# Kernel optimization log

Hardware: AMD Instinct MI355X
Metric: run time of the kernel (lower is better)

Reference implementation:

```python
import jax, jax.numpy as jnp
import numpy as np

B, S, H = 1, 2048, 4096
NQ, NKV, D = 32, 8, 128
N_REP = NQ // NKV
SCALE = 1.0 / np.sqrt(D)
SOFTCAP = 30.0
EPS = 1e-5


def _rotate_half(x):
    x1, x2 = jnp.split(x, 2, axis=-1)
    return jnp.concatenate([-x2, x1], axis=-1)


def _rms_norm(x, w, eps=EPS):
    xf = x.astype(jnp.float32)
    norm = xf * jax.lax.rsqrt(jnp.mean(xf * xf, axis=-1, keepdims=True) + eps)
    return (w * norm).astype(x.dtype)


def setup_inputs() -> dict:
    key = jax.random.key(0)
    ks = jax.random.split(key, 8)
    hidden_states = jax.random.normal(ks[0], (B, S, H), dtype=jnp.float32)
    # causal additive mask
    causal = jnp.tril(jnp.ones((S, S), dtype=bool))
    attention_mask = jnp.where(causal, 0.0, -1e9)[None, None].astype(jnp.float32)
    # RoPE cache
    inv_freq = 1.0 / (10000.0 ** (np.arange(0, D, 2, dtype=np.float32) / D))
    t = np.arange(S, dtype=np.float32)
    freqs = np.outer(t, inv_freq)                      # (S, D/2)
    emb = np.concatenate([freqs, freqs], axis=-1)      # (S, D)
    cos = jnp.asarray(np.cos(emb))[None, None]         # (1,1,S,D)
    sin = jnp.asarray(np.sin(emb))[None, None]
    # params
    std = 0.02
    wq = jax.random.normal(ks[1], (NQ * D, H), dtype=jnp.float32) * std
    wk = jax.random.normal(ks[2], (NKV * D, H), dtype=jnp.float32) * std
    wv = jax.random.normal(ks[3], (NKV * D, H), dtype=jnp.float32) * std
    wo = jax.random.normal(ks[4], (H, NQ * D), dtype=jnp.float32) * std
    pre_norm_w = jnp.ones((H,), dtype=jnp.float32)
    q_norm_w = jnp.ones((D,), dtype=jnp.float32)
    k_norm_w = jnp.ones((D,), dtype=jnp.float32)
    return {
        "hidden_states": hidden_states, "attention_mask": attention_mask,
        "cos": cos, "sin": sin, "pre_norm_w": pre_norm_w,
        "wq": wq, "wk": wk, "wv": wv, "wo": wo,
        "q_norm_w": q_norm_w, "k_norm_w": k_norm_w,
    }


def reference(hidden_states, attention_mask, cos, sin, pre_norm_w,
              wq, wk, wv, wo, q_norm_w, k_norm_w):
    residual = hidden_states
    h = _rms_norm(hidden_states, pre_norm_w)
    bsz, seq_len, _ = h.shape
    # projections -> (b, heads, s, d)
    q = jnp.einsum('bsh,eh->bse', h, wq).reshape(bsz, seq_len, NQ, D).transpose(0, 2, 1, 3)
    k = jnp.einsum('bsh,eh->bse', h, wk).reshape(bsz, seq_len, NKV, D).transpose(0, 2, 1, 3)
    v = jnp.einsum('bsh,eh->bse', h, wv).reshape(bsz, seq_len, NKV, D).transpose(0, 2, 1, 3)
    # QK RMSNorm over head_dim
    q = _rms_norm(q, q_norm_w)
    k = _rms_norm(k, k_norm_w)
    # RoPE (full head_dim)
    q = q * cos + _rotate_half(q) * sin
    k = k * cos + _rotate_half(k) * sin
    # GQA: repeat kv heads
    k_exp = jnp.repeat(k, N_REP, axis=1)  # (b, NQ, s, d)
    v_exp = jnp.repeat(v, N_REP, axis=1)
    scores = jnp.einsum('bhqd,bhkd->bhqk', q, k_exp) * SCALE
    scores = SOFTCAP * jnp.tanh(scores / SOFTCAP)
    scores = scores + attention_mask
    probs = jax.nn.softmax(scores.astype(jnp.float32), axis=-1).astype(q.dtype)
    attn = jnp.einsum('bhqk,bhkd->bhqd', probs, v_exp)
    attn = attn.transpose(0, 2, 1, 3).reshape(bsz, seq_len, NQ * D)
    out = jnp.einsum('bse,he->bsh', attn, wo)
    return residual + out
```

## Files before the change

### kernel.cpp

```cpp
#include <hip/hip_runtime.h>
#include <cstdint>

typedef __bf16 bf16;
typedef __bf16 bf16x8 __attribute__((ext_vector_type(8)));
typedef __bf16 bf16x4 __attribute__((ext_vector_type(4)));
typedef float  f32x4  __attribute__((ext_vector_type(4)));

#define SEQ  2048
#define HID  4096
#define DH   128
#define NQH  32
#define NKVH 8
#define NTOT 6144
#define RSCALE 0.08838834764831845f
#define SOFTCAP 30.0f
#define L2E 1.4426950408889634f

__device__ __forceinline__ void gl2lds16(const void* g, void* l) {
  __builtin_amdgcn_global_load_lds(
      (const __attribute__((address_space(1))) unsigned int*)g,
      (__attribute__((address_space(3))) unsigned int*)l, 16, 0, 0);
}

__global__ void cvt_kernel(const float* __restrict__ in, bf16* __restrict__ out, int n4) {
  const int stride = gridDim.x * blockDim.x;
  for (int i = blockIdx.x * blockDim.x + threadIdx.x; i < n4; i += stride) {
    const float4 v = ((const float4*)in)[i];
    bf16x4 o = { (bf16)v.x, (bf16)v.y, (bf16)v.z, (bf16)v.w };
    *(bf16x4*)(out + (size_t)i * 4) = o;
  }
}

__global__ void rmsnorm_kernel(const float* __restrict__ x, const float* __restrict__ w,
                               bf16* __restrict__ out, float* __restrict__ res_out) {
  const int s = blockIdx.x;
  const float* xr = x + (size_t)s * HID;
  float4 v[4];
  float ss = 0.f;
#pragma unroll
  for (int j = 0; j < 4; ++j) {
    v[j] = ((const float4*)xr)[threadIdx.x + j * 256];
    ss += v[j].x * v[j].x + v[j].y * v[j].y + v[j].z * v[j].z + v[j].w * v[j].w;
  }
#pragma unroll
  for (int m = 1; m < 64; m <<= 1) ss += __shfl_xor(ss, m);
  __shared__ float red[4];
  if ((threadIdx.x & 63) == 0) red[threadIdx.x >> 6] = ss;
  __syncthreads();
  const float rn = rsqrtf((red[0] + red[1] + red[2] + red[3]) * (1.f / HID) + 1e-5f);
  bf16* orow = out + (size_t)s * HID;
  float4* rrow = (float4*)(res_out + (size_t)s * HID);
#pragma unroll
  for (int j = 0; j < 4; ++j) {
    const int idx = (threadIdx.x + j * 256) * 4;
    const float4 wv = ((const float4*)w)[threadIdx.x + j * 256];
    bf16x4 o = { (bf16)(v[j].x * rn * wv.x), (bf16)(v[j].y * rn * wv.y),
                 (bf16)(v[j].z * rn * wv.z), (bf16)(v[j].w * rn * wv.w) };
    *(bf16x4*)(orow + idx) = o;
    rrow[threadIdx.x + j * 256] = v[j];
  }
}

template<bool FINAL>
__global__ __launch_bounds__(512, 1)
void gemmring(const bf16* __restrict__ A, const bf16* __restrict__ B,
              bf16* __restrict__ Cb, float* __restrict__ Cf,
              int M, int N, int Ktot, int Klen)
{
  extern __shared__ char smem[];
  const int tid  = threadIdx.x;
  const int lane = tid & 63;
  const int wave = tid >> 6;
  const int wm = wave >> 2, wn = wave & 3;

  const int gx = gridDim.x;
  const int nwg = gx * gridDim.y;
  int lin = blockIdx.x + gx * blockIdx.y;
  lin = (lin & 7) * (nwg >> 3) + (lin >> 3);
  const int m0 = (lin / gx) * 256;
  const int n0 = (lin % gx) * 256;
  const int k0 = blockIdx.z * Klen;

  const int rsub = lane >> 2;
  const int g8   = (((lane & 3) ^ (rsub & 3))) * 8;
  auto stage = [&](int c, int sl) {
    const int kt = k0 + c * 32;
    char* base = smem + sl * 32768;
#pragma unroll
    for (int l = 0; l < 2; ++l) {
      const int p = wave * 2 + l;
      gl2lds16(A + (size_t)(m0 + p * 16 + rsub) * Ktot + kt + g8, base + p * 1024);
    }
#pragma unroll
    for (int l = 0; l < 2; ++l) {
      const int p = wave * 2 + l;
      gl2lds16(B + (size_t)(n0 + p * 16 + rsub) * Ktot + kt + g8, base + 16384 + p * 1024);
    }
  };

  f32x4 acc[8][4] = {};
  const int n_ch = Klen / 32;

  const int rl = lane & 15;
  const int sw = ((lane >> 4) ^ (lane & 3)) * 8;

  stage(0, 0); stage(1, 1); stage(2, 2); stage(3, 3);
  asm volatile("s_waitcnt vmcnt(12)" ::: "memory");
  asm volatile("s_barrier" ::: "memory");

  int rs = 0, ss = 4;
  for (int c = 0; c < n_ch; ++c) {
    if (c + 4 < n_ch) stage(c + 4, ss);
    const bf16* Ab = (const bf16*)(smem + rs * 32768);
    const bf16* Bb = (const bf16*)(smem + rs * 32768 + 16384);
    bf16x8 afr[8], bfr[4];
#pragma unroll
    for (int mi = 0; mi < 8; ++mi)
      afr[mi] = *(const bf16x8*)(Ab + (wm * 128 + mi * 16 + rl) * 32 + sw);
#pragma unroll
    for (int ni = 0; ni < 4; ++ni)
      bfr[ni] = *(const bf16x8*)(Bb + (wn * 64 + ni * 16 + rl) * 32 + sw);
    asm volatile("s_waitcnt lgkmcnt(0)" ::: "memory");
    __builtin_amdgcn_sched_barrier(0);
    __builtin_amdgcn_s_setprio(1);
#pragma unroll
    for (int mi = 0; mi < 8; ++mi)
#pragma unroll
      for (int ni = 0; ni < 4; ++ni)
        acc[mi][ni] = __builtin_amdgcn_mfma_f32_16x16x32_bf16(afr[mi], bfr[ni], acc[mi][ni], 0, 0, 0);
    __builtin_amdgcn_s_setprio(0);
    if (c + 5 <= n_ch)      { asm volatile("s_waitcnt vmcnt(12)" ::: "memory"); }
    else if (c + 4 == n_ch) { asm volatile("s_waitcnt vmcnt(8)"  ::: "memory"); }
    else if (c + 3 == n_ch) { asm volatile("s_waitcnt vmcnt(4)"  ::: "memory"); }
    else if (c + 2 == n_ch) { asm volatile("s_waitcnt vmcnt(0)"  ::: "memory"); }
    asm volatile("s_barrier" ::: "memory");
    rs = (rs == 4) ? 0 : rs + 1;
    ss = (ss == 4) ? 0 : ss + 1;
  }

#pragma unroll
  for (int mi = 0; mi < 8; ++mi) {
#pragma unroll
    for (int i = 0; i < 4; ++i) {
      const int m = m0 + wm * 128 + mi * 16 + (lane >> 4) * 4 + i;
#pragma unroll
      for (int ni = 0; ni < 4; ++ni) {
        const int n = n0 + wn * 64 + ni * 16 + (lane & 15);
        const float v = acc[mi][ni][i];
        if constexpr (FINAL) {
          atomicAdd(Cf + (size_t)m * N + n, v);
        } else {
          Cb[(size_t)m * N + n] = (bf16)v;
        }
      }
    }
  }
}

__global__ void qkrope_kernel(const bf16* __restrict__ qkv,
                              const float* __restrict__ qw, const float* __restrict__ kw,
                              const float* __restrict__ cs, const float* __restrict__ sn,
                              bf16* __restrict__ qr, bf16* __restrict__ kr)
{
  const int w = blockIdx.x * 4 + (threadIdx.x >> 6);
  const int lane = threadIdx.x & 63;
  const int s = w / (NQH + NKVH);
  const int hh = w % (NQH + NKVH);
  const bf16* src; bf16* dst; const float* nw;
  if (hh < NQH) {
    src = qkv + (size_t)s * NTOT + hh * DH;
    dst = qr + ((size_t)hh * SEQ + s) * DH;
    nw = qw;
  } else {
    const int h2 = hh - NQH;
    src = qkv + (size_t)s * NTOT + 4096 + h2 * DH;
    dst = kr + ((size_t)h2 * SEQ + s) * DH;
    nw = kw;
  }
  const float x0 = (float)src[lane], x1 = (float)src[lane + 64];
  float ss = x0 * x0 + x1 * x1;
#pragma unroll
  for (int m = 1; m < 64; m <<= 1) ss += __shfl_xor(ss, m);
  const float rn = rsqrtf(ss * (1.f / DH) + 1e-5f);
  const float n0 = x0 * rn * nw[lane], n1 = x1 * rn * nw[lane + 64];
  const float c0 = cs[s * DH + lane],      s0 = sn[s * DH + lane];
  const float c1 = cs[s * DH + lane + 64], s1 = sn[s * DH + lane + 64];
  dst[lane]      = (bf16)(n0 * c0 - n1 * s0);
  dst[lane + 64] = (bf16)(n1 * c1 + n0 * s1);
}

__global__ void vtrans_kernel(const bf16* __restrict__ qkv, bf16* __restrict__ vt)
{
  __shared__ bf16 tbuf[64][33];
  const int s0 = blockIdx.x * 64;
  const int d0 = blockIdx.y * 32;
  const int h  = blockIdx.z;
  const int tid = threadIdx.x;
  {
    const int col = tid & 31, r0 = tid >> 5;
    for (int r = r0; r < 64; r += 8)
      tbuf[r][col] = qkv[(size_t)(s0 + r) * NTOT + 5120 + h * DH + d0 + col];
  }
  __syncthreads();
  {
    const int sc = tid & 63, dr0 = tid >> 6;
    for (int d = dr0; d < 32; d += 4)
      vt[((size_t)h * DH + d0 + d) * SEQ + s0 + sc] = tbuf[sc][d];
  }
}

__global__ __launch_bounds__(256, 2)
void attn_kernel(const bf16* __restrict__ Q, const bf16* __restrict__ Kr,
                 const bf16* __restrict__ Vt, bf16* __restrict__ Oa)
{
  __shared__ bf16 Ks[2][64 * 128];
  __shared__ bf16 Vs[2][128 * 64];
  __shared__ bf16 Ps[4][32 * 64];

  const int tid = threadIdx.x, lane = tid & 63, wave = tid >> 6;

  const int lin  = blockIdx.x + 16 * blockIdx.y;
  const int slot = lin >> 8, idx = lin & 255;
  const int bx   = slot ? (15 - (idx & 15)) : (idx & 15);
  const int head = (slot << 4) | (idx >> 4);
  const int kvh  = head >> 2;
  const int q0   = bx * 128;
  const int wq0  = q0 + wave * 32;

  const bf16* Qh = Q  + (size_t)head * SEQ * DH;
  const bf16* Kh = Kr + (size_t)kvh * SEQ * DH;
  const bf16* Vh = Vt + (size_t)kvh * DH * SEQ;

  bf16x8 qf[2][4];
#pragma unroll
  for (int mt = 0; mt < 2; ++mt)
#pragma unroll
    for (int kc = 0; kc < 4; ++kc) {
      const int r = wq0 + mt * 16 + (lane & 15);
      qf[mt][kc] = *(const bf16x8*)(Qh + (size_t)r * DH + kc * 32 + (lane >> 4) * 8);
    }

  float lsum[2][4] = {};
  f32x4 o_acc[2][8] = {};

  const int ntiles = q0 / 64 + 2;

  auto stage = [&](int t, int b) {
    const int kv0 = t * 64;
    bf16* Kd = &Ks[b][0];
    bf16* Vd = &Vs[b][0];
#pragma unroll
    for (int i2 = 0; i2 < 4; ++i2) {
      const int c = wave * 4 + i2;
      {
        const int row = c * 4 + (lane >> 4);
        const int col8 = (lane & 15) ^ (row & 15);
        gl2lds16(Kh + (size_t)(kv0 + row) * DH + col8 * 8, Kd + c * 512);
      }
      {
        const int row = c * 8 + (lane >> 3);
        const int col8 = (lane & 7) ^ (row & 7);
        gl2lds16(Vh + (size_t)row * SEQ + kv0 + col8 * 8, Vd + c * 512);
      }
    }
  };

  stage(0, 0);
  __syncthreads();

  const float ZS = RSCALE / SOFTCAP;
  const float A1 = RSCALE * L2E;
  const float B3 = -(ZS * ZS) * (1.f / 3.f);
  const float B5 = (2.f / 15.f) * (ZS * ZS) * (ZS * ZS);
  const float C  = SOFTCAP * L2E;

  for (int t = 0; t < ntiles; ++t) {
    const int cur = t & 1;
    if (t + 1 < ntiles) stage(t + 1, cur ^ 1);
    const int kv0 = t * 64;
    const bf16* Kb = &Ks[cur][0];
    const bf16* Vb = &Vs[cur][0];

    if (kv0 <= wq0 + 31) {
      f32x4 sc[2][4] = {};
      __builtin_amdgcn_s_setprio(1);
#pragma unroll
      for (int ks = 0; ks < 4; ++ks) {
        bf16x8 kf[4];
#pragma unroll
        for (int nt = 0; nt < 4; ++nt) {
          const int row = nt * 16 + (lane & 15);
          const int sl = (ks * 4 + (lane >> 4)) ^ (row & 15);
          kf[nt] = *(const bf16x8*)(Kb + row * 128 + sl * 8);
        }
#pragma unroll
        for (int mt = 0; mt < 2; ++mt)
#pragma unroll
          for (int nt = 0; nt < 4; ++nt)
            sc[mt][nt] = __builtin_amdgcn_mfma_f32_16x16x32_bf16(qf[mt][ks], kf[nt], sc[mt][nt], 0, 0, 0);
      }
      __builtin_amdgcn_s_setprio(0);

      if (kv0 + 63 <= wq0) {
#pragma unroll
        for (int mt = 0; mt < 2; ++mt)
#pragma unroll
          for (int i = 0; i < 4; ++i)
#pragma unroll
            for (int nt = 0; nt < 4; ++nt) {
              const float s = sc[mt][nt][i];
              const float w = s * s;
              const float poly = fmaf(fmaf(B5, w, B3), w, 1.f);
              const float p = __builtin_amdgcn_exp2f(fmaf(s * poly, A1, -C));
              sc[mt][nt][i] = p;
              lsum[mt][i] += p;
            }
      } else {
#pragma unroll
        for (int mt = 0; mt < 2; ++mt)
#pragma unroll
          for (int i = 0; i < 4; ++i) {
            const int qrow = wq0 + mt * 16 + (lane >> 4) * 4 + i;
#pragma unroll
            for (int nt = 0; nt < 4; ++nt) {
              const int col = kv0 + nt * 16 + (lane & 15);
              const float s = sc[mt][nt][i];
              const float w = s * s;
              const float poly = fmaf(fmaf(B5, w, B3), w, 1.f);
              float p = __builtin_amdgcn_exp2f(fmaf(s * poly, A1, -C));
              if (col > qrow) p = 0.f;
              sc[mt][nt][i] = p;
              lsum[mt][i] += p;
            }
          }
      }

#pragma unroll
      for (int mt = 0; mt < 2; ++mt)
#pragma unroll
        for (int nt = 0; nt < 4; ++nt)
#pragma unroll
          for (int i = 0; i < 4; ++i) {
            const int r = mt * 16 + (lane >> 4) * 4 + i;
            const int colb = nt * 16 + (lane & 15);
            const int sl = (colb >> 3) ^ (r & 7);
            Ps[wave][r * 64 + sl * 8 + (colb & 7)] = (bf16)sc[mt][nt][i];
          }
      asm volatile("s_waitcnt lgkmcnt(0)" ::: "memory");
      __builtin_amdgcn_sched_barrier(0);

      __builtin_amdgcn_s_setprio(1);
#pragma unroll
      for (int ks2 = 0; ks2 < 2; ++ks2) {
        bf16x8 pf[2];
#pragma unroll
        for (int mt = 0; mt < 2; ++mt) {
          const int r = mt * 16 + (lane & 15);
          const int sl = (ks2 * 4 + (lane >> 4)) ^ (r & 7);
          pf[mt] = *(const bf16x8*)(&Ps[wave][r * 64 + sl * 8]);
        }
#pragma unroll
        for (int nt = 0; nt < 8; ++nt) {
          const int row = nt * 16 + (lane & 15);
          const int sl = (ks2 * 4 + (lane >> 4)) ^ (row & 7);
          const bf16x8 vf = *(const bf16x8*)(Vb + row * 64 + sl * 8);
          o_acc[0][nt] = __builtin_amdgcn_mfma_f32_16x16x32_bf16(pf[0], vf, o_acc[0][nt], 0, 0, 0);
          o_acc[1][nt] = __builtin_amdgcn_mfma_f32_16x16x32_bf16(pf[1], vf, o_acc[1][nt], 0, 0, 0);
        }
      }
      __builtin_amdgcn_s_setprio(0);
    }
    __syncthreads();
  }

#pragma unroll
  for (int mt = 0; mt < 2; ++mt)
#pragma unroll
    for (int i = 0; i < 4; ++i) {
      float l = lsum[mt][i];
#pragma unroll
      for (int m = 1; m < 16; m <<= 1) l += __shfl_xor(l, m);
      const int qrow = wq0 + mt * 16 + (lane >> 4) * 4 + i;
      const float inv_l = 1.f / l;
#pragma unroll
      for (int nt = 0; nt < 8; ++nt) {
        const int d = nt * 16 + (lane & 15);
        Oa[(size_t)qrow * HID + head * DH + d] = (bf16)(o_acc[mt][nt][i] * inv_l);
      }
    }
}

extern "C" void kernel_launch(void* const* d_in, const int* in_sizes, int n_in,
                              void* d_out, int out_size, void* d_ws, size_t ws_size,
                              hipStream_t stream)
{
  const float* hidden = (const float*)d_in[0];
  const float* cosb   = (const float*)d_in[2];
  const float* sinb   = (const float*)d_in[3];
  const float* prew   = (const float*)d_in[4];
  const float* wq     = (const float*)d_in[5];
  const float* wk     = (const float*)d_in[6];
  const float* wv     = (const float*)d_in[7];
  const float* wo     = (const float*)d_in[8];
  const float* qnw    = (const float*)d_in[9];
  const float* knw    = (const float*)d_in[10];
  float* outp = (float*)d_out;
  char* ws = (char*)d_ws;

  bf16* wqkv = (bf16*)(ws + 0);
  bf16* hb   = (bf16*)(ws + 50331648);
  bf16* qkvp = (bf16*)(ws + 67108864);
  bf16* kr   = (bf16*)(ws + 92274688);
  bf16* vt   = (bf16*)(ws + 96468992);
  bf16* wob  = wqkv;

  cvt_kernel<<<2048, 256, 0, stream>>>(wq, wqkv, 4096 * HID / 4);
  cvt_kernel<<<1024, 256, 0, stream>>>(wk, wqkv + (size_t)4096 * HID, 1024 * HID / 4);
  cvt_kernel<<<1024, 256, 0, stream>>>(wv, wqkv + (size_t)5120 * HID, 1024 * HID / 4);
  rmsnorm_kernel<<<SEQ, 256, 0, stream>>>(hidden, prew, hb, outp);

  gemmring<false><<<dim3(NTOT / 256, SEQ / 256, 1), 512, 163840, stream>>>(
      hb, wqkv, qkvp, nullptr, SEQ, NTOT, HID, HID);

  cvt_kernel<<<2048, 256, 0, stream>>>(wo, wob, HID * HID / 4);

  qkrope_kernel<<<SEQ * (NQH + NKVH) / 4, 256, 0, stream>>>(qkvp, qnw, knw, cosb, sinb, hb, kr);
  vtrans_kernel<<<dim3(32, 4, 8), 256, 0, stream>>>(qkvp, vt);

  attn_kernel<<<dim3(16, 32), 256, 0, stream>>>(hb, kr, vt, qkvp);

  gemmring<true><<<dim3(HID / 256, SEQ / 256, 2), 512, 163840, stream>>>(
      qkvp, wob, nullptr, outp, SEQ, HID, HID, HID / 2);
}
```

Measured before the change: 399.2 us.

## Restructure GEMM into double-buffered 64-wide K tiles with interleaved quarter staging

```diff
diff --git a/kernel.cpp b/kernel.cpp
--- a/kernel.cpp
+++ b/kernel.cpp
@@ -62,10 +62,10 @@
 }
 
 template<bool FINAL>
-__global__ __launch_bounds__(512, 1)
-void gemmring(const bf16* __restrict__ A, const bf16* __restrict__ B,
-              bf16* __restrict__ Cb, float* __restrict__ Cf,
-              int M, int N, int Ktot, int Klen)
+__global__ __launch_bounds__(512, 2)
+void gemm8p(const bf16* __restrict__ A, const bf16* __restrict__ B,
+            bf16* __restrict__ Cb, float* __restrict__ Cf,
+            int M, int N, int Ktot, int Klen)
 {
   extern __shared__ char smem[];
   const int tid  = threadIdx.x;
@@ -81,61 +81,84 @@
   const int n0 = (lin % gx) * 256;
   const int k0 = blockIdx.z * Klen;
 
-  const int rsub = lane >> 2;
-  const int g8   = (((lane & 3) ^ (rsub & 3))) * 8;
-  auto stage = [&](int c, int sl) {
-    const int kt = k0 + c * 32;
-    char* base = smem + sl * 32768;
+  auto stageH = [&](int kt, int slot, int h) {
+    const bf16* src = (h & 2) ? (B + (size_t)n0 * Ktot) : (A + (size_t)m0 * Ktot);
+    char* base = smem + slot * 65536 + (h & 2) * 16384 + (h & 1) * 16384;
+    const int r0 = (h & 1) * 128;
 #pragma unroll
     for (int l = 0; l < 2; ++l) {
-      const int p = wave * 2 + l;
-      gl2lds16(A + (size_t)(m0 + p * 16 + rsub) * Ktot + kt + g8, base + p * 1024);
-    }
-#pragma unroll
-    for (int l = 0; l < 2; ++l) {
-      const int p = wave * 2 + l;
-      gl2lds16(B + (size_t)(n0 + p * 16 + rsub) * Ktot + kt + g8, base + 16384 + p * 1024);
+      const int c = wave * 2 + l;
+      const int row = r0 + c * 8 + (lane >> 3);
+      const int col8 = (lane & 7) ^ (row & 7);
+      gl2lds16(src + (size_t)row * Ktot + kt + col8 * 8,
+               base + (size_t)c * 1024);
     }
   };
 
   f32x4 acc[8][4] = {};
-  const int n_ch = Klen / 32;
-
-  const int rl = lane & 15;
-  const int sw = ((lane >> 4) ^ (lane & 3)) * 8;
-
-  stage(0, 0); stage(1, 1); stage(2, 2); stage(3, 3);
-  asm volatile("s_waitcnt vmcnt(12)" ::: "memory");
+  const int nk = Klen / 64;
+  const int rl = lane & 15, hi = lane >> 4;
+
+#pragma unroll
+  for (int h = 0; h < 4; ++h) stageH(k0, 0, h);
+#pragma unroll
+  for (int h = 0; h < 4; ++h) stageH(k0 + 64, 1, h);
+  asm volatile("s_waitcnt vmcnt(0)" ::: "memory");
   asm volatile("s_barrier" ::: "memory");
 
-  int rs = 0, ss = 4;
-  for (int c = 0; c < n_ch; ++c) {
-    if (c + 4 < n_ch) stage(c + 4, ss);
-    const bf16* Ab = (const bf16*)(smem + rs * 32768);
-    const bf16* Bb = (const bf16*)(smem + rs * 32768 + 16384);
-    bf16x8 afr[8], bfr[4];
-#pragma unroll
-    for (int mi = 0; mi < 8; ++mi)
-      afr[mi] = *(const bf16x8*)(Ab + (wm * 128 + mi * 16 + rl) * 32 + sw);
-#pragma unroll
-    for (int ni = 0; ni < 4; ++ni)
-      bfr[ni] = *(const bf16x8*)(Bb + (wn * 64 + ni * 16 + rl) * 32 + sw);
-    asm volatile("s_waitcnt lgkmcnt(0)" ::: "memory");
-    __builtin_amdgcn_sched_barrier(0);
-    __builtin_amdgcn_s_setprio(1);
-#pragma unroll
-    for (int mi = 0; mi < 8; ++mi)
-#pragma unroll
-      for (int ni = 0; ni < 4; ++ni)
-        acc[mi][ni] = __builtin_amdgcn_mfma_f32_16x16x32_bf16(afr[mi], bfr[ni], acc[mi][ni], 0, 0, 0);
-    __builtin_amdgcn_s_setprio(0);
-    if (c + 5 <= n_ch)      { asm volatile("s_waitcnt vmcnt(12)" ::: "memory"); }
-    else if (c + 4 == n_ch) { asm volatile("s_waitcnt vmcnt(8)"  ::: "memory"); }
-    else if (c + 3 == n_ch) { asm volatile("s_waitcnt vmcnt(4)"  ::: "memory"); }
-    else if (c + 2 == n_ch) { asm volatile("s_waitcnt vmcnt(0)"  ::: "memory"); }
-    asm volatile("s_barrier" ::: "memory");
-    rs = (rs == 4) ? 0 : rs + 1;
-    ss = (ss == 4) ? 0 : ss + 1;
+  for (int k = 0; k < nk; ++k) {
+    const int slot = k & 1;
+    const bf16* Aa = (const bf16*)(smem + slot * 65536);
+    const bf16* Ba = (const bf16*)(smem + slot * 65536 + 32768);
+    const int kt = k0 + k * 64;
+    bf16x8 bfr[4][2];
+
+#pragma unroll
+    for (int q = 0; q < 4; ++q) {
+      bf16x8 afr[2][2];
+#pragma unroll
+      for (int mi = 0; mi < 2; ++mi)
+#pragma unroll
+        for (int ks = 0; ks < 2; ++ks) {
+          const int row = wm * 128 + q * 32 + mi * 16 + rl;
+          const int slt = (ks * 4 + hi) ^ (row & 7);
+          afr[mi][ks] = *(const bf16x8*)(Aa + row * 64 + slt * 8);
+        }
+      if (q == 0) {
+#pragma unroll
+        for (int ni = 0; ni < 4; ++ni)
+#pragma unroll
+          for (int ks = 0; ks < 2; ++ks) {
+            const int row = wn * 64 + ni * 16 + rl;
+            const int slt = (ks * 4 + hi) ^ (row & 7);
+            bfr[ni][ks] = *(const bf16x8*)(Ba + row * 64 + slt * 8);
+          }
+      }
+      if (q == 0 && k + 1 < nk) stageH(kt + 64,  (k + 1) & 1, 0);
+      if (q == 1 && k + 1 < nk) stageH(kt + 64,  (k + 1) & 1, 1);
+      if (q == 2 && k + 2 < nk) stageH(kt + 128, slot, 2);
+      if (q == 3 && k + 2 < nk) stageH(kt + 128, slot, 3);
+
+      asm volatile("s_barrier" ::: "memory");
+      asm volatile("s_waitcnt lgkmcnt(0)" ::: "memory");
+      __builtin_amdgcn_sched_barrier(0);
+      __builtin_amdgcn_s_setprio(1);
+#pragma unroll
+      for (int ks = 0; ks < 2; ++ks)
+#pragma unroll
+        for (int mi = 0; mi < 2; ++mi)
+#pragma unroll
+          for (int ni = 0; ni < 4; ++ni)
+            acc[q * 2 + mi][ni] = __builtin_amdgcn_mfma_f32_16x16x32_bf16(
+                afr[mi][ks], bfr[ni][ks], acc[q * 2 + mi][ni], 0, 0, 0);
+      __builtin_amdgcn_s_setprio(0);
+
+      if (q == 3) {
+        if (k + 2 < nk)      { asm volatile("s_waitcnt vmcnt(4)" ::: "memory"); }
+        else if (k + 1 < nk) { asm volatile("s_waitcnt vmcnt(0)" ::: "memory"); }
+      }
+      asm volatile("s_barrier" ::: "memory");
+    }
   }
 
 #pragma unroll
@@ -419,7 +442,7 @@
   cvt_kernel<<<1024, 256, 0, stream>>>(wv, wqkv + (size_t)5120 * HID, 1024 * HID / 4);
   rmsnorm_kernel<<<SEQ, 256, 0, stream>>>(hidden, prew, hb, outp);
 
-  gemmring<false><<<dim3(NTOT / 256, SEQ / 256, 1), 512, 163840, stream>>>(
+  gemm8p<false><<<dim3(NTOT / 256, SEQ / 256, 1), 512, 131072, stream>>>(
       hb, wqkv, qkvp, nullptr, SEQ, NTOT, HID, HID);
 
   cvt_kernel<<<2048, 256, 0, stream>>>(wo, wob, HID * HID / 4);
@@ -429,6 +452,6 @@
 
   attn_kernel<<<dim3(16, 32), 256, 0, stream>>>(hb, kr, vt, qkvp);
 
-  gemmring<true><<<dim3(HID / 256, SEQ / 256, 2), 512, 163840, stream>>>(
+  gemm8p<true><<<dim3(HID / 256, SEQ / 256, 2), 512, 131072, stream>>>(
       qkvp, wob, nullptr, outp, SEQ, HID, HID, HID / 2);
 }
```

Result: no change. 391.6 us (-1.9%).
